# Kernel tuning notes

Measured on AMD Instinct MI355X. Metric: run time of the kernel, lower is better.

The kernel has to match this reference:

```python
import jax, jax.numpy as jnp
import numpy as np

B = 131072          # batch of VAD triples
NUM_CLASSES = 10    # number of per-label projection blocks
OUT_DIM = 768       # embedding dim
IN_DIM = 3          # VAD dim


def setup_inputs() -> dict:
    key = jax.random.key(0)
    k1, k2, k3 = jax.random.split(key, 3)
    vad = jax.random.normal(k1, (B, IN_DIM), dtype=jnp.float32)
    labels = jax.random.randint(k2, (B,), 0, NUM_CLASSES, dtype=jnp.int32)
    # stacked W_blocks: (num_classes, output_dim, input_dim)
    W = jax.random.normal(k3, (NUM_CLASSES, OUT_DIM, IN_DIM), dtype=jnp.float32)
    return {"vad": vad, "labels": labels, "W": W}


def reference(vad, labels, W):
    # Batched version of: for v in vad: emb = v @ W_blocks[label].T
    W_sel = W[labels]                       # (B, out, in) gather of expert blocks
    out = jnp.einsum("bod,bd->bo", W_sel, vad)  # (B, out) tiny per-sample matvec
    return out
```

## Files before the change

### kernel.cpp

```cpp
#include <hip/hip_runtime.h>


#define B_TOTAL 131072
#define OUT_DIM 768

__global__ __launch_bounds__(256) void vad_proj_kernel(
    const float* __restrict__ vad,
    const int*   __restrict__ labels,
    const float* __restrict__ W,
    float*       __restrict__ out)
{
    const int lane = threadIdx.x & 63;
    const int wave_in_block = __builtin_amdgcn_readfirstlane((int)(threadIdx.x >> 6));
    const int waves_per_block = blockDim.x >> 6;
    const int nwaves = gridDim.x * waves_per_block;
    int b = blockIdx.x * waves_per_block + wave_in_block;

    #pragma unroll 2
    for (; b < B_TOTAL; b += nwaves) {
        const int l = labels[b];
        const float* vb = vad + (size_t)b * 3;
        const float v0 = vb[0], v1 = vb[1], v2 = vb[2];

        const float4* wbase = (const float4*)(W + (size_t)l * (OUT_DIM * 3));
        float4* obase = (float4*)(out + (size_t)b * OUT_DIM);

        #pragma unroll
        for (int k = 0; k < 3; ++k) {
            const int q = lane + 64 * k;
            const float4 w0 = wbase[q * 3 + 0];
            const float4 w1 = wbase[q * 3 + 1];
            const float4 w2 = wbase[q * 3 + 2];
            float4 o;
            o.x = w0.x * v0 + w0.y * v1 + w0.z * v2;
            o.y = w0.w * v0 + w1.x * v1 + w1.y * v2;
            o.z = w1.z * v0 + w1.w * v1 + w2.x * v2;
            o.w = w2.y * v0 + w2.z * v1 + w2.w * v2;
            obase[q] = o;
        }
    }
}

extern "C" void kernel_launch(void* const* d_in, const int* in_sizes, int n_in,
                              void* d_out, int out_size, void* d_ws, size_t ws_size,
                              hipStream_t stream) {
    const float* vad    = (const float*)d_in[0];
    const int*   labels = (const int*)d_in[1];
    const float* W      = (const float*)d_in[2];
    float*       out    = (float*)d_out;

    vad_proj_kernel<<<2048, 256, 0, stream>>>(vad, labels, W, out);
}
```

Measured before the change: 84.48 us.

## Stage transposed weights in LDS and use nontemporal output stores

Each block loads the full 10x768x3 weight tensor into shared memory, transposed to a d-major layout so each lane reads contiguous float4 rows per input dim. Weight gathers then come from LDS instead of L2/global. Output writes switch to nontemporal stores, and the launch changes to 256 blocks of 1024 threads, each owning a fixed contiguous sample range. The cost is a 92KB LDS footprint per block that limits occupancy, plus a per-block preload with integer division work.

```diff
diff --git a/kernel.cpp b/kernel.cpp
--- a/kernel.cpp
+++ b/kernel.cpp
@@ -1,42 +1,60 @@
 #include <hip/hip_runtime.h>
 
 
+typedef float f32x4 __attribute__((ext_vector_type(4)));
+
 #define B_TOTAL 131072
 #define OUT_DIM 768
+#define NCLS 10
+#define W_ELEMS (NCLS * OUT_DIM * 3)
+#define BLOCK 1024
+#define GRID 256
+#define SAMPLES_PER_BLOCK (B_TOTAL / GRID)
+#define WAVES_PER_BLOCK (BLOCK / 64)
+#define SAMPLES_PER_WAVE (SAMPLES_PER_BLOCK / WAVES_PER_BLOCK)
 
-__global__ __launch_bounds__(256) void vad_proj_kernel(
+__global__ __launch_bounds__(BLOCK) void vad_proj_kernel(
     const float* __restrict__ vad,
     const int*   __restrict__ labels,
     const float* __restrict__ W,
     float*       __restrict__ out)
 {
-    const int lane = threadIdx.x & 63;
-    const int wave_in_block = __builtin_amdgcn_readfirstlane((int)(threadIdx.x >> 6));
-    const int waves_per_block = blockDim.x >> 6;
-    const int nwaves = gridDim.x * waves_per_block;
-    int b = blockIdx.x * waves_per_block + wave_in_block;
+    __shared__ float wlds[W_ELEMS];
+
+    const int tid = threadIdx.x;
+
+    for (int g = tid; g < W_ELEMS; g += BLOCK) {
+        const float val = W[g];
+        const int l   = g / (OUT_DIM * 3);
+        const int rem = g - l * (OUT_DIM * 3);
+        const int o   = rem / 3;
+        const int d   = rem - o * 3;
+        wlds[l * (OUT_DIM * 3) + d * OUT_DIM + o] = val;
+    }
+    __syncthreads();
+
+    const int lane = tid & 63;
+    const int wave = __builtin_amdgcn_readfirstlane(tid >> 6);
+    const int b0 = blockIdx.x * SAMPLES_PER_BLOCK + wave;
 
     #pragma unroll 2
-    for (; b < B_TOTAL; b += nwaves) {
+    for (int j = 0; j < SAMPLES_PER_WAVE; ++j) {
+        const int b = b0 + j * WAVES_PER_BLOCK;
         const int l = labels[b];
         const float* vb = vad + (size_t)b * 3;
         const float v0 = vb[0], v1 = vb[1], v2 = vb[2];
 
-        const float4* wbase = (const float4*)(W + (size_t)l * (OUT_DIM * 3));
-        float4* obase = (float4*)(out + (size_t)b * OUT_DIM);
+        const float* base = wlds + l * (OUT_DIM * 3);
+        f32x4* obase = (f32x4*)(out + (size_t)b * OUT_DIM);
 
         #pragma unroll
         for (int k = 0; k < 3; ++k) {
             const int q = lane + 64 * k;
-            const float4 w0 = wbase[q * 3 + 0];
-            const float4 w1 = wbase[q * 3 + 1];
-            const float4 w2 = wbase[q * 3 + 2];
-            float4 o;
-            o.x = w0.x * v0 + w0.y * v1 + w0.z * v2;
-            o.y = w0.w * v0 + w1.x * v1 + w1.y * v2;
-            o.z = w1.z * v0 + w1.w * v1 + w2.x * v2;
-            o.w = w2.y * v0 + w2.z * v1 + w2.w * v2;
-            obase[q] = o;
+            const f32x4 wd0 = *(const f32x4*)(base + 0 * OUT_DIM + 4 * q);
+            const f32x4 wd1 = *(const f32x4*)(base + 1 * OUT_DIM + 4 * q);
+            const f32x4 wd2 = *(const f32x4*)(base + 2 * OUT_DIM + 4 * q);
+            f32x4 o = wd0 * v0 + wd1 * v1 + wd2 * v2;
+            __builtin_nontemporal_store(o, obase + q);
         }
     }
 }
@@ -49,5 +67,5 @@
     const float* W      = (const float*)d_in[2];
     float*       out    = (float*)d_out;
 
-    vad_proj_kernel<<<2048, 256, 0, stream>>>(vad, labels, W, out);
+    vad_proj_kernel<<<GRID, BLOCK, 0, stream>>>(vad, labels, W, out);
 }
```

New measurement: 86.50 us. 1.02x slower.

## Keep all class weight slices in registers and select per sample

Applied to the files above, without the earlier changes.

Each thread now preloads its slice of all ten class weight blocks into registers (120 floats) once. It then loops over samples assigned to its block, choosing the weight set with a uniform switch on the label. This removes the per-sample gather of weights from cache and leaves the kernel bound by output writes. The cost is much higher register pressure, which lowers occupancy, plus a serial 64-sample loop per block with 3-wave blocks.

```diff
diff --git a/kernel.cpp b/kernel.cpp
--- a/kernel.cpp
+++ b/kernel.cpp
@@ -1,43 +1,53 @@
 #include <hip/hip_runtime.h>
 
 
+typedef float f32x4 __attribute__((ext_vector_type(4)));
+
 #define B_TOTAL 131072
 #define OUT_DIM 768
+#define NCLS 10
+#define GRID 2048
+#define BLOCK 192
+#define SAMPLES_PER_BLOCK (B_TOTAL / GRID)
 
-__global__ __launch_bounds__(256) void vad_proj_kernel(
+__global__ __launch_bounds__(BLOCK) void vad_proj_kernel(
     const float* __restrict__ vad,
     const int*   __restrict__ labels,
     const float* __restrict__ W,
     float*       __restrict__ out)
 {
     const int lane = threadIdx.x & 63;
-    const int wave_in_block = __builtin_amdgcn_readfirstlane((int)(threadIdx.x >> 6));
-    const int waves_per_block = blockDim.x >> 6;
-    const int nwaves = gridDim.x * waves_per_block;
-    int b = blockIdx.x * waves_per_block + wave_in_block;
+    const int wv   = __builtin_amdgcn_readfirstlane((int)(threadIdx.x >> 6));
+    const int q    = lane + (wv << 6);
 
-    #pragma unroll 2
-    for (; b < B_TOTAL; b += nwaves) {
+    f32x4 w[NCLS][3];
+    #pragma unroll
+    for (int c = 0; c < NCLS; ++c) {
+        const f32x4* wp = (const f32x4*)(W + (size_t)c * (OUT_DIM * 3)) + q * 3;
+        w[c][0] = wp[0]; w[c][1] = wp[1]; w[c][2] = wp[2];
+    }
+
+    for (int j = 0; j < SAMPLES_PER_BLOCK; ++j) {
+        const int b = blockIdx.x + j * GRID;
         const int l = labels[b];
         const float* vb = vad + (size_t)b * 3;
         const float v0 = vb[0], v1 = vb[1], v2 = vb[2];
 
-        const float4* wbase = (const float4*)(W + (size_t)l * (OUT_DIM * 3));
-        float4* obase = (float4*)(out + (size_t)b * OUT_DIM);
+        f32x4 o;
+        switch (l) {
+#define CASE(c) case c: { \
+            const f32x4 a0 = w[c][0], a1 = w[c][1], a2 = w[c][2]; \
+            o.x = a0.x*v0 + a0.y*v1 + a0.z*v2; \
+            o.y = a0.w*v0 + a1.x*v1 + a1.y*v2; \
+            o.z = a1.z*v0 + a1.w*v1 + a2.x*v2; \
+            o.w = a2.y*v0 + a2.z*v1 + a2.w*v2; } break;
+            CASE(0) CASE(1) CASE(2) CASE(3) CASE(4)
+            CASE(5) CASE(6) CASE(7) CASE(8) CASE(9)
+#undef CASE
+            default: o = (f32x4)(0.0f); break;
+        }
 
-        #pragma unroll
-        for (int k = 0; k < 3; ++k) {
-            const int q = lane + 64 * k;
-            const float4 w0 = wbase[q * 3 + 0];
-            const float4 w1 = wbase[q * 3 + 1];
-            const float4 w2 = wbase[q * 3 + 2];
-            float4 o;
-            o.x = w0.x * v0 + w0.y * v1 + w0.z * v2;
-            o.y = w0.w * v0 + w1.x * v1 + w1.y * v2;
-            o.z = w1.z * v0 + w1.w * v1 + w2.x * v2;
-            o.w = w2.y * v0 + w2.z * v1 + w2.w * v2;
-            obase[q] = o;
-        }
+        ((f32x4*)(out + (size_t)b * OUT_DIM))[q] = o;
     }
 }
 
@@ -49,5 +59,5 @@
     const float* W      = (const float*)d_in[2];
     float*       out    = (float*)d_out;
 
-    vad_proj_kernel<<<2048, 256, 0, stream>>>(vad, labels, W, out);
+    vad_proj_kernel<<<GRID, BLOCK, 0, stream>>>(vad, labels, W, out);
 }
```

Result: slower. 156.7 us (+85.5%).
